# Kernel optimization log

Hardware: AMD Instinct MI355X
Metric: run time of the kernel (lower is better)

## Reference

```python
import jax, jax.numpy as jnp
import numpy as np

N = 50000
E = 800000
IN_C, HID_C, OUT_C = 128, 256, 2


def sage_conv(x, src, dst, W_l, b_l, W_r, num_nodes):
    # PyG SAGEConv with mean aggregation:
    #   out = lin_l(mean_{j in N(i)} x_j) + lin_r(x_i)
    msg = x[src]                                            # [E, d] gather
    agg = jax.ops.segment_sum(msg, dst, num_segments=num_nodes)   # [N, d]
    cnt = jax.ops.segment_sum(jnp.ones((msg.shape[0],), x.dtype), dst,
                              num_segments=num_nodes)        # [N]
    agg = agg / jnp.maximum(cnt, 1.0)[:, None]               # mean (deg>=1)
    return agg @ W_l.T + b_l + x @ W_r.T


def setup_inputs() -> dict:
    key = jax.random.key(0)
    ks = jax.random.split(key, 8)
    x = jax.random.normal(ks[0], (N, IN_C), dtype=jnp.float32)
    edge_index = jax.random.randint(ks[1], (2, E), 0, N, dtype=jnp.int32)
    # glorot-ish scaled params
    s1 = 1.0 / np.sqrt(IN_C)
    s2 = 1.0 / np.sqrt(HID_C)
    W1l = jax.random.normal(ks[2], (HID_C, IN_C), dtype=jnp.float32) * s1
    W1r = jax.random.normal(ks[3], (HID_C, IN_C), dtype=jnp.float32) * s1
    b1 = jnp.zeros((HID_C,), dtype=jnp.float32)
    W2l = jax.random.normal(ks[4], (OUT_C, HID_C), dtype=jnp.float32) * s2
    W2r = jax.random.normal(ks[5], (OUT_C, HID_C), dtype=jnp.float32) * s2
    b2 = jnp.zeros((OUT_C,), dtype=jnp.float32)
    return {"x": x, "edge_index": edge_index,
            "W1l": W1l, "b1": b1, "W1r": W1r,
            "W2l": W2l, "b2": b2, "W2r": W2r}


def reference(x, edge_index, W1l, b1, W1r, W2l, b2, W2r):
    src, dst = edge_index[0], edge_index[1]
    h = sage_conv(x, src, dst, W1l, b1, W1r, N)
    h = jax.nn.relu(h)
    out = sage_conv(h, src, dst, W2l, b2, W2r, N)
    return out
```

## Files before the change

kernel.cpp:

```cpp
#include <hip/hip_runtime.h>
#include <hip/hip_bf16.h>


#define IN_C 128
#define HID_C 256
#define BKT_SHIFT 7
#define BKT_W 128
#define CAP 3072

typedef __attribute__((ext_vector_type(8))) short short8;
typedef __attribute__((ext_vector_type(4))) float f32x4;

static __device__ __forceinline__ unsigned short f2b(float f) {
    __hip_bfloat16 h = __float2bfloat16(f);
    return *(unsigned short*)&h;
}
static __device__ __forceinline__ float b2f(unsigned short u) {
    unsigned v = ((unsigned)u) << 16;
    return *(float*)&v;
}

__global__ __launch_bounds__(512) void scatter_conv(
    const float* __restrict__ x, unsigned int* __restrict__ xh,
    unsigned int* __restrict__ Abf,
    const float* __restrict__ w1l, const float* __restrict__ w1r,
    unsigned short* __restrict__ Bg,
    const int* __restrict__ ei, int* __restrict__ bcnt,
    unsigned int* __restrict__ binned,
    int npairs , int xblk, int E_) {
    __shared__ int hist[512];
    __shared__ int lbase[512];
    const int tid = threadIdx.x;
    if (blockIdx.x < xblk) {
        int t = blockIdx.x * 512 + tid;
        if (t >= npairs) return;
        float2 v = *(const float2*)&x[(size_t)t * 2];
        unsigned int o = ((unsigned)f2b(v.y) << 16) | f2b(v.x);
        xh[t] = o;
        int node = t >> 6, g = t & 63;
        Abf[(size_t)node * 128 + 64 + g] = o;
    } else if (blockIdx.x < xblk + 128) {
        int idx = (blockIdx.x - xblk) * 512 + tid;
        int o = idx >> 8, k = idx & 255;
        float f = (k < IN_C) ? w1l[o * IN_C + k] : w1r[o * IN_C + (k - IN_C)];
        Bg[idx] = f2b(f);
    } else {
        const int e0 = (blockIdx.x - xblk - 128) * 2048;
        hist[tid] = 0;
        __syncthreads();
#pragma unroll
        for (int j = 0; j < 4; ++j) {
            int e = e0 + j * 512 + tid;
            if (e < E_) atomicAdd(&hist[ei[E_ + e] >> BKT_SHIFT], 1);
        }
        __syncthreads();
        {
            int c = hist[tid];
            lbase[tid] = c ? tid * CAP + atomicAdd(&bcnt[tid], c) : 0;
            hist[tid] = 0;
        }
        __syncthreads();
#pragma unroll
        for (int j = 0; j < 4; ++j) {
            int e = e0 + j * 512 + tid;
            if (e < E_) {
                int d = ei[E_ + e];
                int b = d >> BKT_SHIFT;
                int pos = lbase[b] + atomicAdd(&hist[b], 1);
                if (pos < b * CAP + CAP)
                    binned[pos] = ((unsigned)ei[e] << BKT_SHIFT) |
                                  (unsigned)(d & (BKT_W - 1));
            }
        }
    }
}


__global__ __launch_bounds__(1024) void sort_gather(
    const unsigned int* __restrict__ binned, const int* __restrict__ bcnt,
    const uint4* __restrict__ xh4, uint4* __restrict__ Abf4,
    int* __restrict__ deg, int n) {
    __shared__ unsigned int ebuf[CAP];
    __shared__ unsigned short sbuf[CAP];
    __shared__ int hist[BKT_W];
    __shared__ int offs[BKT_W];
    __shared__ int cur[BKT_W];
    const int tid = threadIdx.x;
    const int lane = tid & 63;
    const int bkt = blockIdx.x;
    const int gbase = bkt * CAP;
    int cnt = bcnt[bkt];
    if (cnt > CAP) cnt = CAP;

    if (tid < BKT_W) hist[tid] = 0;
    for (int i = tid; i < cnt; i += 1024) ebuf[i] = binned[gbase + i];
    __syncthreads();
    for (int i = tid; i < cnt; i += 1024)
        atomicAdd(&hist[ebuf[i] & (BKT_W - 1)], 1);
    __syncthreads();
    if (tid < 64) {
        int h0 = hist[lane * 2], h1 = hist[lane * 2 + 1];
        int s = h0 + h1;
        int incl = s;
#pragma unroll
        for (int off = 1; off < 64; off <<= 1) {
            int t = __shfl_up(incl, off);
            if (lane >= off) incl += t;
        }
        int excl = incl - s;
        offs[lane * 2] = excl;          cur[lane * 2] = excl;
        offs[lane * 2 + 1] = excl + h0; cur[lane * 2 + 1] = excl + h0;
    }
    __syncthreads();
    for (int i = tid; i < cnt; i += 1024) {
        unsigned int pk = ebuf[i];
        int pos = atomicAdd(&cur[pk & (BKT_W - 1)], 1);
        sbuf[pos] = (unsigned short)(pk >> BKT_SHIFT);
    }
    if (tid < BKT_W) {
        int node = bkt * BKT_W + tid;
        if (node < n) deg[node] = hist[tid];
    }
    __syncthreads();

    const int wv = tid >> 6;
    const int ep = lane >> 4;
    const int pos = lane & 15;
    for (int ld = wv * 8; ld < wv * 8 + 8; ++ld) {
        int node = bkt * BKT_W + ld;
        if (node >= n) break;
        int beg = offs[ld], end = offs[ld] + hist[ld];
        float s[8] = {0.f, 0.f, 0.f, 0.f, 0.f, 0.f, 0.f, 0.f};
        for (int e = beg; e < end; e += 8) {
#pragma unroll
            for (int g = 0; g < 2; ++g) {
                int eg = e + g * 4 + ep;
                if (eg < end) {
                    int src = sbuf[eg];
                    uint4 u = xh4[(size_t)src * 16 + pos];
                    s[0] += b2f(u.x & 0xffff); s[1] += b2f(u.x >> 16);
                    s[2] += b2f(u.y & 0xffff); s[3] += b2f(u.y >> 16);
                    s[4] += b2f(u.z & 0xffff); s[5] += b2f(u.z >> 16);
                    s[6] += b2f(u.w & 0xffff); s[7] += b2f(u.w >> 16);
                }
            }
        }
#pragma unroll
        for (int i = 0; i < 8; ++i) {
            s[i] += __shfl_xor(s[i], 16);
            s[i] += __shfl_xor(s[i], 32);
        }
        if (ep == 0) {
            float inv = 1.0f / (float)max(end - beg, 1);
            uint4 o;
            o.x = ((unsigned)f2b(s[1] * inv) << 16) | f2b(s[0] * inv);
            o.y = ((unsigned)f2b(s[3] * inv) << 16) | f2b(s[2] * inv);
            o.z = ((unsigned)f2b(s[5] * inv) << 16) | f2b(s[4] * inv);
            o.w = ((unsigned)f2b(s[7] * inv) << 16) | f2b(s[6] * inv);
            Abf4[(size_t)node * 32 + pos] = o;
        }
    }
}


#define LSTR 72

__global__ __launch_bounds__(256) void gemm1_fused(
    const unsigned short* __restrict__ Abf, const unsigned short* __restrict__ Bg,
    const float* __restrict__ b1, const float* __restrict__ w2l,
    const float* __restrict__ w2r, float* __restrict__ pr_part, int nn) {
    __shared__ short As[128 * LSTR];
    __shared__ short Bs[128 * LSTR];

    const int tid = threadIdx.x;
    const int lane = tid & 63;
    const int wid = tid >> 6;
    const int wm = wid >> 1, wn = wid & 1;
    const int row0 = blockIdx.x * 128;
    const int col0 = blockIdx.y * 128;

    const int srow = tid >> 1;
    const int skc = (tid & 1) * 32;
    int arow = row0 + srow;
    if (arow >= nn) arow = nn - 1;
    const size_t agoff = (size_t)arow * 256 + skc;
    const size_t bgoff = (size_t)(col0 + srow) * 256 + skc;

    f32x4 acc[4][4];
#pragma unroll
    for (int i = 0; i < 4; ++i)
#pragma unroll
        for (int j = 0; j < 4; ++j) acc[i][j] = (f32x4){0.f, 0.f, 0.f, 0.f};

    const int quad = lane >> 4;
    const int l16 = lane & 15;

    for (int k0 = 0; k0 < 256; k0 += 64) {
        const uint4* ga = (const uint4*)(Abf + agoff + k0);
        const uint4* gb = (const uint4*)(Bg + bgoff + k0);
        uint4 va0 = ga[0], va1 = ga[1], va2 = ga[2], va3 = ga[3];
        uint4 vb0 = gb[0], vb1 = gb[1], vb2 = gb[2], vb3 = gb[3];

        __syncthreads();
        uint4* la = (uint4*)&As[srow * LSTR + skc];
        uint4* lb = (uint4*)&Bs[srow * LSTR + skc];
        la[0] = va0; la[1] = va1; la[2] = va2; la[3] = va3;
        lb[0] = vb0; lb[1] = vb1; lb[2] = vb2; lb[3] = vb3;
        __syncthreads();

#pragma unroll
        for (int kb = 0; kb < 2; ++kb) {
            short8 af[4], bf[4];
#pragma unroll
            for (int mt = 0; mt < 4; ++mt)
                af[mt] = *(const short8*)&As[(wm * 64 + mt * 16 + l16) * LSTR + kb * 32 + quad * 8];
#pragma unroll
            for (int nt = 0; nt < 4; ++nt)
                bf[nt] = *(const short8*)&Bs[(wn * 64 + nt * 16 + l16) * LSTR + kb * 32 + quad * 8];
#pragma unroll
            for (int mt = 0; mt < 4; ++mt)
#pragma unroll
                for (int nt = 0; nt < 4; ++nt)
                    acc[mt][nt] = __builtin_amdgcn_mfma_f32_16x16x32_bf16(
                        af[mt], bf[nt], acc[mt][nt], 0, 0, 0);
        }
    }

    const int cbase = col0 + wn * 64 + l16;
    const int cby = blockIdx.y * 2 + wn;
#pragma unroll
    for (int half = 0; half < 2; ++half) {
        const float* wA = half ? w2r : w2l;
        f32x4 part[2][4];
#pragma unroll
        for (int c = 0; c < 2; ++c)
#pragma unroll
            for (int mt = 0; mt < 4; ++mt) part[c][mt] = (f32x4){0.f, 0.f, 0.f, 0.f};
#pragma unroll
        for (int nt = 0; nt < 4; ++nt) {
            const int col = cbase + nt * 16;
            const float bias = b1[col];
            const float w0 = wA[col];
            const float w1 = wA[HID_C + col];
#pragma unroll
            for (int mt = 0; mt < 4; ++mt)
#pragma unroll
                for (int r = 0; r < 4; ++r) {
                    float hv = fmaxf(acc[mt][nt][r] + bias, 0.0f);
                    part[0][mt][r] += hv * w0;
                    part[1][mt][r] += hv * w1;
                }
        }
#pragma unroll
        for (int c = 0; c < 2; ++c)
#pragma unroll
            for (int mt = 0; mt < 4; ++mt)
#pragma unroll
                for (int r = 0; r < 4; ++r)
#pragma unroll
                    for (int m = 1; m < 16; m <<= 1)
                        part[c][mt][r] += __shfl_xor(part[c][mt][r], m);
        if (l16 < 8) {
            const int ch2 = l16 & 1;
            const int mts = l16 >> 1;
#pragma unroll
            for (int r = 0; r < 4; ++r) {
                int row = row0 + wm * 64 + quad * 4 + mts * 16 + r;
                if (row < nn)
                    pr_part[(size_t)row * 16 + cby * 4 + half * 2 + ch2] =
                        part[ch2][mts][r];
            }
        }
    }
}


__global__ void combine2(const float* __restrict__ pr_part,
                         float2* __restrict__ p2, float2* __restrict__ rs, int n) {
    int i = blockIdx.x * 256 + threadIdx.x;
    if (i >= n) return;
    const float4* q = (const float4*)(pr_part + (size_t)i * 16);
    float4 a = q[0], b = q[1], c = q[2], d = q[3];
    p2[i] = make_float2(a.x + b.x + c.x + d.x, a.y + b.y + c.y + d.y);
    rs[i] = make_float2(a.z + b.z + c.z + d.z, a.w + b.w + c.w + d.w);
}

__global__ __launch_bounds__(256) void fin_bucket(
    const unsigned int* __restrict__ binned, const int* __restrict__ bcnt,
    const float2* __restrict__ p2, const float2* __restrict__ rs,
    const int* __restrict__ deg, const float* __restrict__ b2,
    float* __restrict__ out, int n) {
    __shared__ float a0[BKT_W];
    __shared__ float a1[BKT_W];
    const int tid = threadIdx.x;
    const int bkt = blockIdx.x;
    const int gbase = bkt * CAP;
    int cnt = bcnt[bkt];
    if (cnt > CAP) cnt = CAP;
    if (tid < BKT_W) { a0[tid] = 0.0f; a1[tid] = 0.0f; }
    __syncthreads();
    for (int i = tid; i < cnt; i += 256) {
        unsigned pk = binned[gbase + i];
        float2 v = p2[pk >> BKT_SHIFT];
        atomicAdd(&a0[pk & (BKT_W - 1)], v.x);
        atomicAdd(&a1[pk & (BKT_W - 1)], v.y);
    }
    __syncthreads();
    if (tid < BKT_W) {
        int node = bkt * BKT_W + tid;
        if (node < n) {
            float inv = 1.0f / (float)max(deg[node], 1);
            float2 self = rs[node];
            out[node * 2 + 0] = a0[tid] * inv + self.x + b2[0];
            out[node * 2 + 1] = a1[tid] * inv + self.y + b2[1];
        }
    }
}


extern "C" void kernel_launch(void* const* d_in, const int* in_sizes, int n_in,
                              void* d_out, int out_size, void* d_ws, size_t ws_size,
                              hipStream_t stream) {
    const float* x   = (const float*)d_in[0];
    const int*   ei  = (const int*)d_in[1];
    const float* W1l = (const float*)d_in[2];
    const float* b1  = (const float*)d_in[3];
    const float* W1r = (const float*)d_in[4];
    const float* W2l = (const float*)d_in[5];
    const float* b2  = (const float*)d_in[6];
    const float* W2r = (const float*)d_in[7];
    float* out = (float*)d_out;

    const int N_ = in_sizes[0] / IN_C;
    const int E_ = in_sizes[1] / 2;
    const int nbkt = (N_ + BKT_W - 1) / BKT_W;

    char* wsb = (char*)d_ws;
    size_t off = 0;
    auto alloc = [&](size_t bytes) {
        void* ptr = wsb + off;
        off += ((bytes + 15) & ~(size_t)15);
        return ptr;
    };
    unsigned short* Abf = (unsigned short*)alloc((size_t)N_ * 256 * 2);
    unsigned int*   xh  = (unsigned int*)alloc((size_t)N_ * 64 * 4);
    unsigned short* Bg  = (unsigned short*)alloc(256 * 256 * 2);
    float* pr_part = (float*)alloc((size_t)N_ * 16 * 4);
    unsigned int* binned = (unsigned int*)alloc((size_t)(nbkt + 1) * CAP * 4);
    int*   bcnt   = (int*)alloc(512 * 4);
    int*   deg    = (int*)alloc((size_t)N_ * 4);
    float2* p2 = (float2*)alloc((size_t)N_ * 2 * 4);
    float2* rs = (float2*)alloc((size_t)N_ * 2 * 4);

    const int xblk = (N_ * 64 + 511) / 512;
    const int eblk = (E_ + 2047) / 2048;

    hipMemsetAsync(bcnt, 0, 512 * sizeof(int), stream);
    scatter_conv<<<xblk + 128 + eblk, 512, 0, stream>>>(
        x, xh, (unsigned int*)Abf, W1l, W1r, Bg, ei, bcnt, binned,
        N_ * 64, xblk, E_);

    sort_gather<<<nbkt, 1024, 0, stream>>>(binned, bcnt, (const uint4*)xh,
                                           (uint4*)Abf, deg, N_);

    gemm1_fused<<<dim3((N_ + 127) / 128, 2), 256, 0, stream>>>(
        Abf, Bg, b1, W2l, W2r, pr_part, N_);

    combine2<<<(N_ + 255) / 256, 256, 0, stream>>>(pr_part, p2, rs, N_);
    fin_bucket<<<nbkt, 256, 0, stream>>>(binned, bcnt, p2, rs, deg, b2, out, N_);
}
```

Baseline: 191.5 us.

## Drop xh copy and combine kernel; reuse sorted edges in final aggregation

Removes the separate bf16 copy of x and gathers neighbour features directly from the self half of the A buffer. The gemm epilogue now atomically accumulates the layer-2 projections into zeroed arrays, so the combine2 kernel and its partial buffer are gone. sort_gather writes the per-bucket sorted source list and node offsets back to global memory, letting fin_bucket do a per-node segmented sum with no shared-memory atomics. The edge loader also keeps destination indices in registers instead of reading them twice. In exchange, float atomics to global memory make the sums order-dependent, and the gather and write of the same A buffer within sort_gather relies on the self half and the aggregate half not overlapping.

New measurement: 185.3 us. 1.03x faster.

```diff
diff --git a/kernel.cpp b/kernel.cpp
--- a/kernel.cpp
+++ b/kernel.cpp
@@ -21,8 +21,7 @@
 }
 
 __global__ __launch_bounds__(512) void scatter_conv(
-    const float* __restrict__ x, unsigned int* __restrict__ xh,
-    unsigned int* __restrict__ Abf,
+    const float* __restrict__ x, unsigned int* __restrict__ Abf,
     const float* __restrict__ w1l, const float* __restrict__ w1r,
     unsigned short* __restrict__ Bg,
     const int* __restrict__ ei, int* __restrict__ bcnt,
@@ -36,7 +35,6 @@
         if (t >= npairs) return;
         float2 v = *(const float2*)&x[(size_t)t * 2];
         unsigned int o = ((unsigned)f2b(v.y) << 16) | f2b(v.x);
-        xh[t] = o;
         int node = t >> 6, g = t & 63;
         Abf[(size_t)node * 128 + 64 + g] = o;
     } else if (blockIdx.x < xblk + 128) {
@@ -48,10 +46,12 @@
         const int e0 = (blockIdx.x - xblk - 128) * 2048;
         hist[tid] = 0;
         __syncthreads();
+        int dreg[4];
 #pragma unroll
         for (int j = 0; j < 4; ++j) {
             int e = e0 + j * 512 + tid;
-            if (e < E_) atomicAdd(&hist[ei[E_ + e] >> BKT_SHIFT], 1);
+            dreg[j] = (e < E_) ? ei[E_ + e] : -1;
+            if (dreg[j] >= 0) atomicAdd(&hist[dreg[j] >> BKT_SHIFT], 1);
         }
         __syncthreads();
         {
@@ -63,8 +63,8 @@
 #pragma unroll
         for (int j = 0; j < 4; ++j) {
             int e = e0 + j * 512 + tid;
-            if (e < E_) {
-                int d = ei[E_ + e];
+            if (dreg[j] >= 0) {
+                int d = dreg[j];
                 int b = d >> BKT_SHIFT;
                 int pos = lbase[b] + atomicAdd(&hist[b], 1);
                 if (pos < b * CAP + CAP)
@@ -77,9 +77,9 @@
 
 
 __global__ __launch_bounds__(1024) void sort_gather(
-    const unsigned int* __restrict__ binned, const int* __restrict__ bcnt,
-    const uint4* __restrict__ xh4, uint4* __restrict__ Abf4,
-    int* __restrict__ deg, int n) {
+    unsigned int* __restrict__ binned, const int* __restrict__ bcnt,
+    const uint4* __restrict__ abf4c, uint4* __restrict__ Abf4,
+    int* __restrict__ deg, int* __restrict__ boffs, int n) {
     __shared__ unsigned int ebuf[CAP];
     __shared__ unsigned short sbuf[CAP];
     __shared__ int hist[BKT_W];
@@ -119,9 +119,14 @@
     }
     if (tid < BKT_W) {
         int node = bkt * BKT_W + tid;
-        if (node < n) deg[node] = hist[tid];
-    }
-    __syncthreads();
+        if (node < n) { deg[node] = hist[tid]; boffs[node] = offs[tid]; }
+    }
+    __syncthreads();
+
+    {
+        unsigned short* sout = (unsigned short*)(binned + gbase);
+        for (int i = tid; i < cnt; i += 1024) sout[i] = sbuf[i];
+    }
 
     const int wv = tid >> 6;
     const int ep = lane >> 4;
@@ -137,7 +142,7 @@
                 int eg = e + g * 4 + ep;
                 if (eg < end) {
                     int src = sbuf[eg];
-                    uint4 u = xh4[(size_t)src * 16 + pos];
+                    uint4 u = abf4c[(size_t)src * 32 + 16 + pos];
                     s[0] += b2f(u.x & 0xffff); s[1] += b2f(u.x >> 16);
                     s[2] += b2f(u.y & 0xffff); s[3] += b2f(u.y >> 16);
                     s[4] += b2f(u.z & 0xffff); s[5] += b2f(u.z >> 16);
@@ -168,7 +173,8 @@
 __global__ __launch_bounds__(256) void gemm1_fused(
     const unsigned short* __restrict__ Abf, const unsigned short* __restrict__ Bg,
     const float* __restrict__ b1, const float* __restrict__ w2l,
-    const float* __restrict__ w2r, float* __restrict__ pr_part, int nn) {
+    const float* __restrict__ w2r, float* __restrict__ p2g,
+    float* __restrict__ rsg, int nn) {
     __shared__ short As[128 * LSTR];
     __shared__ short Bs[128 * LSTR];
 
@@ -227,10 +233,10 @@
     }
 
     const int cbase = col0 + wn * 64 + l16;
-    const int cby = blockIdx.y * 2 + wn;
 #pragma unroll
     for (int half = 0; half < 2; ++half) {
         const float* wA = half ? w2r : w2l;
+        float* og = half ? rsg : p2g;
         f32x4 part[2][4];
 #pragma unroll
         for (int c = 0; c < 2; ++c)
@@ -267,53 +273,46 @@
             for (int r = 0; r < 4; ++r) {
                 int row = row0 + wm * 64 + quad * 4 + mts * 16 + r;
                 if (row < nn)
-                    pr_part[(size_t)row * 16 + cby * 4 + half * 2 + ch2] =
-                        part[ch2][mts][r];
+                    atomicAdd(&og[row * 2 + ch2], part[ch2][mts][r]);
             }
         }
     }
 }
 
 
-__global__ void combine2(const float* __restrict__ pr_part,
-                         float2* __restrict__ p2, float2* __restrict__ rs, int n) {
-    int i = blockIdx.x * 256 + threadIdx.x;
-    if (i >= n) return;
-    const float4* q = (const float4*)(pr_part + (size_t)i * 16);
-    float4 a = q[0], b = q[1], c = q[2], d = q[3];
-    p2[i] = make_float2(a.x + b.x + c.x + d.x, a.y + b.y + c.y + d.y);
-    rs[i] = make_float2(a.z + b.z + c.z + d.z, a.w + b.w + c.w + d.w);
-}
-
 __global__ __launch_bounds__(256) void fin_bucket(
-    const unsigned int* __restrict__ binned, const int* __restrict__ bcnt,
+    const unsigned int* __restrict__ binned, const int* __restrict__ boffs,
+    const int* __restrict__ deg,
     const float2* __restrict__ p2, const float2* __restrict__ rs,
-    const int* __restrict__ deg, const float* __restrict__ b2,
-    float* __restrict__ out, int n) {
-    __shared__ float a0[BKT_W];
-    __shared__ float a1[BKT_W];
+    const float* __restrict__ b2, float* __restrict__ out, int n) {
+    __shared__ float ps0[BKT_W];
+    __shared__ float ps1[BKT_W];
     const int tid = threadIdx.x;
+    const int ln = tid & (BKT_W - 1);
+    const int hp = tid >> 7;
     const int bkt = blockIdx.x;
-    const int gbase = bkt * CAP;
-    int cnt = bcnt[bkt];
-    if (cnt > CAP) cnt = CAP;
-    if (tid < BKT_W) { a0[tid] = 0.0f; a1[tid] = 0.0f; }
-    __syncthreads();
-    for (int i = tid; i < cnt; i += 256) {
-        unsigned pk = binned[gbase + i];
-        float2 v = p2[pk >> BKT_SHIFT];
-        atomicAdd(&a0[pk & (BKT_W - 1)], v.x);
-        atomicAdd(&a1[pk & (BKT_W - 1)], v.y);
-    }
-    __syncthreads();
-    if (tid < BKT_W) {
-        int node = bkt * BKT_W + tid;
-        if (node < n) {
-            float inv = 1.0f / (float)max(deg[node], 1);
-            float2 self = rs[node];
-            out[node * 2 + 0] = a0[tid] * inv + self.x + b2[0];
-            out[node * 2 + 1] = a1[tid] * inv + self.y + b2[1];
-        }
+    const int node = bkt * BKT_W + ln;
+    const unsigned short* sp =
+        (const unsigned short*)(binned + (size_t)bkt * CAP);
+    float s0 = 0.f, s1 = 0.f;
+    int dg = 0;
+    if (node < n) {
+        int beg = boffs[node];
+        dg = deg[node];
+        int end = beg + dg;
+        for (int i = beg + hp; i < end; i += 2) {
+            float2 v = p2[sp[i]];
+            s0 += v.x; s1 += v.y;
+        }
+    }
+    if (hp) { ps0[ln] = s0; ps1[ln] = s1; }
+    __syncthreads();
+    if (!hp && node < n) {
+        s0 += ps0[ln]; s1 += ps1[ln];
+        float inv = 1.0f / (float)max(dg, 1);
+        float2 self = rs[node];
+        out[node * 2 + 0] = s0 * inv + self.x + b2[0];
+        out[node * 2 + 1] = s1 * inv + self.y + b2[1];
     }
 }
 
@@ -343,29 +342,30 @@
         return ptr;
     };
     unsigned short* Abf = (unsigned short*)alloc((size_t)N_ * 256 * 2);
-    unsigned int*   xh  = (unsigned int*)alloc((size_t)N_ * 64 * 4);
     unsigned short* Bg  = (unsigned short*)alloc(256 * 256 * 2);
-    float* pr_part = (float*)alloc((size_t)N_ * 16 * 4);
     unsigned int* binned = (unsigned int*)alloc((size_t)(nbkt + 1) * CAP * 4);
-    int*   bcnt   = (int*)alloc(512 * 4);
-    int*   deg    = (int*)alloc((size_t)N_ * 4);
-    float2* p2 = (float2*)alloc((size_t)N_ * 2 * 4);
-    float2* rs = (float2*)alloc((size_t)N_ * 2 * 4);
+    int*   bcnt = (int*)alloc(512 * 4);
+    float* p2f  = (float*)alloc((size_t)N_ * 2 * 4);
+    float* rsf  = (float*)alloc((size_t)N_ * 2 * 4);
+    int*   deg  = (int*)alloc((size_t)N_ * 4);
+    int*   boffs = (int*)alloc((size_t)N_ * 4);
 
     const int xblk = (N_ * 64 + 511) / 512;
     const int eblk = (E_ + 2047) / 2048;
 
-    hipMemsetAsync(bcnt, 0, 512 * sizeof(int), stream);
+    hipMemsetAsync(bcnt, 0, 512 * sizeof(int) + (size_t)N_ * 2 * 4 * 2, stream);
+
     scatter_conv<<<xblk + 128 + eblk, 512, 0, stream>>>(
-        x, xh, (unsigned int*)Abf, W1l, W1r, Bg, ei, bcnt, binned,
+        x, (unsigned int*)Abf, W1l, W1r, Bg, ei, bcnt, binned,
         N_ * 64, xblk, E_);
 
-    sort_gather<<<nbkt, 1024, 0, stream>>>(binned, bcnt, (const uint4*)xh,
-                                           (uint4*)Abf, deg, N_);
+    sort_gather<<<nbkt, 1024, 0, stream>>>(binned, bcnt, (const uint4*)Abf,
+                                           (uint4*)Abf, deg, boffs, N_);
 
     gemm1_fused<<<dim3((N_ + 127) / 128, 2), 256, 0, stream>>>(
-        Abf, Bg, b1, W2l, W2r, pr_part, N_);
-
-    combine2<<<(N_ + 255) / 256, 256, 0, stream>>>(pr_part, p2, rs, N_);
-    fin_bucket<<<nbkt, 256, 0, stream>>>(binned, bcnt, p2, rs, deg, b2, out, N_);
-}
+        Abf, Bg, b1, W2l, W2r, p2f, rsf, N_);
+
+    fin_bucket<<<nbkt, 256, 0, stream>>>(binned, boffs, deg,
+                                         (const float2*)p2f, (const float2*)rsf,
+                                         b2, out, N_);
+}
```
